# Kernel tuning notes

Measured on AMD Instinct MI355X. Metric: run time of the kernel, lower is better.

The kernel has to match this reference:

```python
import jax, jax.numpy as jnp
import numpy as np


def setup_inputs() -> dict:
    key = jax.random.key(0)
    k1, k2, k3, k4, k5 = jax.random.split(key, 5)
    B, Te, Td, De, Dd = 8, 256, 256, 512, 512
    return {
        "encoder_out_seq": jax.random.normal(k1, (B, Te, De), dtype=jnp.float32),
        "decoder_out_seq": jax.random.normal(k2, (B, Td, Dd), dtype=jnp.float32),
        "W_a": jax.random.normal(k3, (De, De), dtype=jnp.float32) * 0.05,
        "U_a": jax.random.normal(k4, (Dd, De), dtype=jnp.float32) * 0.05,
        "V_a": jax.random.normal(k5, (De, 1), dtype=jnp.float32) * 0.05,
    }


def reference(encoder_out_seq, decoder_out_seq, W_a, U_a, V_a):
    # Bahdanau additive attention, fully vectorized over decoder timesteps
    # (replaces the two sequential K.rnn scans in the original).
    Ws = jnp.einsum('bte,ef->btf', encoder_out_seq, W_a)   # [B,Te,De]
    Uh = jnp.einsum('bqd,df->bqf', decoder_out_seq, U_a)   # [B,Td,De]
    # scores[b,q,t] = tanh(Ws[b,t,:] + Uh[b,q,:]) . V_a
    scores = jnp.einsum('bqtf,f->bqt',
                        jnp.tanh(Ws[:, None, :, :] + Uh[:, :, None, :]),
                        V_a[:, 0])                          # [B,Td,Te]
    e = jax.nn.softmax(scores, axis=-1)                     # attention weights
    c = jnp.einsum('bqt,btf->bqf', e, encoder_out_seq)      # context vectors
    return (c, e)
```

## Files before the change

kernel.cpp:

```cpp
#include <hip/hip_runtime.h>

#define NB 8
#define TE 256
#define TD 256
#define DE 512
#define QT 4

#define K2SCALE 2.8853900817779268f

typedef short bf16x8 __attribute__((ext_vector_type(8)));
typedef float f32x4 __attribute__((ext_vector_type(4)));
typedef unsigned short u16x8 __attribute__((ext_vector_type(8)));

static __device__ __forceinline__ unsigned short f2bf(float x) {
  unsigned int u = __float_as_uint(x);
  u += 0x7fffu + ((u >> 16) & 1u);
  return (unsigned short)(u >> 16);
}

static __device__ __forceinline__ void split8(
    const float4& x0, const float4& x1, u16x8& h, u16x8& l) {
  float xs[8] = {x0.x, x0.y, x0.z, x0.w, x1.x, x1.y, x1.z, x1.w};
  #pragma unroll
  for (int j = 0; j < 8; ++j) {
    unsigned short hh = f2bf(xs[j]);
    float hf = __uint_as_float((unsigned int)hh << 16);
    h[j] = hh;
    l[j] = f2bf(xs[j] - hf);
  }
}

__global__ __launch_bounds__(256) void convB(
    const float* __restrict__ w0, unsigned short* __restrict__ h0, unsigned short* __restrict__ l0,
    const float* __restrict__ w1, unsigned short* __restrict__ h1, unsigned short* __restrict__ l1)
{
  const float* W = blockIdx.z ? w1 : w0;
  unsigned short* H = blockIdx.z ? h1 : h0;
  unsigned short* L = blockIdx.z ? l1 : l0;
  __shared__ unsigned short sh[32][33], sl[32][33];
  const int t = threadIdx.x;
  const int k0 = blockIdx.y * 32, n0 = blockIdx.x * 32;
  const int r = t >> 3, c = (t & 7) * 4;
  float4 x = *(const float4*)(W + (size_t)(k0 + r) * DE + n0 + c);
  float xs[4] = {x.x, x.y, x.z, x.w};
  #pragma unroll
  for (int j = 0; j < 4; ++j) {
    unsigned short hh = f2bf(xs[j]);
    float hf = __uint_as_float((unsigned int)hh << 16);
    sh[r][c + j] = hh;
    sl[r][c + j] = f2bf(xs[j] - hf);
  }
  __syncthreads();
  ushort4 oh, ol;
  oh.x = sh[c + 0][r]; oh.y = sh[c + 1][r]; oh.z = sh[c + 2][r]; oh.w = sh[c + 3][r];
  ol.x = sl[c + 0][r]; ol.y = sl[c + 1][r]; ol.z = sl[c + 2][r]; ol.w = sl[c + 3][r];
  *(ushort4*)(H + (size_t)(n0 + r) * DE + k0 + c) = oh;
  *(ushort4*)(L + (size_t)(n0 + r) * DE + k0 + c) = ol;
}

__global__ __launch_bounds__(256) void gemm_mfma(
    const float* __restrict__ A0,
    const unsigned short* __restrict__ BH0, const unsigned short* __restrict__ BL0,
    float* __restrict__ C0,
    const float* __restrict__ A1,
    const unsigned short* __restrict__ BH1, const unsigned short* __restrict__ BL1,
    float* __restrict__ C1)
{
  const int blk = blockIdx.x;
  const int xcd = blk & 7;
  const int j = blk >> 3;
  const int panel = xcd * 8 + (j & 7);
  const int bx = j >> 3;
  const int by = panel & 31;
  const int bz = panel >> 5;
  const float*          A  = bz ? A1  : A0;
  const unsigned short* BH = bz ? BH1 : BH0;
  const unsigned short* BL = bz ? BL1 : BL0;
  float*                C  = bz ? C1  : C0;
  const int tid  = threadIdx.x;
  const int lane = tid & 63;
  const int wave = tid >> 6;
  const int wm = wave >> 1, wn = wave & 1;
  const int g = lane >> 4, r16 = lane & 15;
  const int m0 = by * 64, n0 = bx * 64;
  __shared__ __align__(16) unsigned short Ah[2][64][40], Al[2][64][40];
  __shared__ __align__(16) unsigned short Bh[2][64][40], Bl[2][64][40];
  const int arow = tid >> 2;
  const int apart = (tid & 3) * 8;

  float4 a00, a01;
  u16x8 pb, plb;
#define LOADTILE(KT) do {                                                   \
    const size_t ko = (size_t)(KT) * 32 + apart;                            \
    const float* pa_ = A + (size_t)(m0 + arow) * 512 + ko;                  \
    a00 = *(const float4*)pa_;  a01 = *(const float4*)(pa_ + 4);            \
    pb  = *(const u16x8*)(BH + (size_t)(n0 + arow) * 512 + ko);             \
    plb = *(const u16x8*)(BL + (size_t)(n0 + arow) * 512 + ko);             \
  } while (0)
#define STORETILE(BUF) do {                                                 \
    u16x8 h0_, l0_;                                                         \
    split8(a00, a01, h0_, l0_);                                             \
    *(u16x8*)&Ah[BUF][arow][apart] = h0_;                                   \
    *(u16x8*)&Al[BUF][arow][apart] = l0_;                                   \
    *(u16x8*)&Bh[BUF][arow][apart] = pb;                                    \
    *(u16x8*)&Bl[BUF][arow][apart] = plb;                                   \
  } while (0)

  f32x4 accm[2][2], acce[2][2];
  #pragma unroll
  for (int mt = 0; mt < 2; ++mt)
    #pragma unroll
    for (int nt = 0; nt < 2; ++nt) {
      accm[mt][nt] = (f32x4){0.f, 0.f, 0.f, 0.f};
      acce[mt][nt] = (f32x4){0.f, 0.f, 0.f, 0.f};
    }

  LOADTILE(0);
  STORETILE(0);
  __syncthreads();

  for (int kt = 0; kt < 16; ++kt) {
    const int cur = kt & 1;
    if (kt + 1 < 16) LOADTILE(kt + 1);
    bf16x8 ah[2], al[2], bh[2], bl[2];
    #pragma unroll
    for (int mt = 0; mt < 2; ++mt) {
      ah[mt] = *(const bf16x8*)&Ah[cur][wm * 32 + mt * 16 + r16][g * 8];
      al[mt] = *(const bf16x8*)&Al[cur][wm * 32 + mt * 16 + r16][g * 8];
    }
    #pragma unroll
    for (int nt = 0; nt < 2; ++nt) {
      bh[nt] = *(const bf16x8*)&Bh[cur][wn * 32 + nt * 16 + r16][g * 8];
      bl[nt] = *(const bf16x8*)&Bl[cur][wn * 32 + nt * 16 + r16][g * 8];
    }
    #pragma unroll
    for (int mt = 0; mt < 2; ++mt)
      #pragma unroll
      for (int nt = 0; nt < 2; ++nt) {
        accm[mt][nt] = __builtin_amdgcn_mfma_f32_16x16x32_bf16(ah[mt], bh[nt], accm[mt][nt], 0, 0, 0);
        acce[mt][nt] = __builtin_amdgcn_mfma_f32_16x16x32_bf16(al[mt], bh[nt], acce[mt][nt], 0, 0, 0);
        acce[mt][nt] = __builtin_amdgcn_mfma_f32_16x16x32_bf16(ah[mt], bl[nt], acce[mt][nt], 0, 0, 0);
      }
    if (kt + 1 < 16) STORETILE(cur ^ 1);
    __syncthreads();
  }
#undef LOADTILE
#undef STORETILE

  #pragma unroll
  for (int mt = 0; mt < 2; ++mt)
    #pragma unroll
    for (int nt = 0; nt < 2; ++nt)
      #pragma unroll
      for (int jj = 0; jj < 4; ++jj) {
        float vsum = accm[mt][nt][jj] + acce[mt][nt][jj];
        int row = m0 + wm * 32 + mt * 16 + g * 4 + jj;
        int col = n0 + wn * 32 + nt * 16 + r16;
        C[(size_t)row * 512 + col] = __builtin_amdgcn_exp2f(vsum * K2SCALE);
      }
}

__global__ __launch_bounds__(512) void attn(
    const float* __restrict__ ws, const float* __restrict__ uh,
    const float* __restrict__ enc, const float* __restrict__ va,
    float* __restrict__ out_c, float* __restrict__ out_e)
{
  const int tid  = threadIdx.x;
  const int wave = tid >> 6;
  const int lane = tid & 63;
  const int b  = blockIdx.x & 7;
  const int q0 = (blockIdx.x >> 3) * QT;
  __shared__ float s_sc[QT][TE];
  __shared__ float red[3][QT][DE];
  const int fbase = lane * 8;

  float4 v0 = *(const float4*)(va + fbase);
  float4 v1 = *(const float4*)(va + fbase + 4);
  float v[8] = {v0.x, v0.y, v0.z, v0.w, v1.x, v1.y, v1.z, v1.w};

  float eu[QT][8];
  #pragma unroll
  for (int q = 0; q < QT; ++q) {
    const float* up = uh + (size_t)(b * TD + q0 + q) * DE + fbase;
    float4 u0 = *(const float4*)(up);
    float4 u1 = *(const float4*)(up + 4);
    eu[q][0] = u0.x; eu[q][1] = u0.y; eu[q][2] = u0.z; eu[q][3] = u0.w;
    eu[q][4] = u1.x; eu[q][5] = u1.y; eu[q][6] = u1.z; eu[q][7] = u1.w;
  }

  const int t0 = wave * 32;
  const float* wp = ws + (size_t)(b * TE + t0) * DE + fbase;
  float4 w0 = *(const float4*)(wp);
  float4 w1 = *(const float4*)(wp + 4);
  for (int t = t0; t < t0 + 32; ++t) {
    float cw[8] = {w0.x, w0.y, w0.z, w0.w, w1.x, w1.y, w1.z, w1.w};
    wp += DE;
    w0 = *(const float4*)(wp);
    w1 = *(const float4*)(wp + 4);
    float a[QT];
    #pragma unroll
    for (int q = 0; q < QT; ++q) {
      float A0 = fmaf(cw[0], eu[q][0], 1.f);
      float A1 = fmaf(cw[1], eu[q][1], 1.f);
      float A2 = fmaf(cw[2], eu[q][2], 1.f);
      float A3 = fmaf(cw[3], eu[q][3], 1.f);
      float B0 = fmaf(cw[4], eu[q][4], 1.f);
      float B1 = fmaf(cw[5], eu[q][5], 1.f);
      float B2 = fmaf(cw[6], eu[q][6], 1.f);
      float B3 = fmaf(cw[7], eu[q][7], 1.f);
      float n1 = fmaf(v[1], A0, v[0] * A1);
      float d1 = A0 * A1;
      float n2 = fmaf(v[3], A2, v[2] * A3);
      float d2 = A2 * A3;
      float N1 = fmaf(n2, d1, n1 * d2);
      float D1 = d1 * d2;
      float n3 = fmaf(v[5], B0, v[4] * B1);
      float d3 = B0 * B1;
      float n4 = fmaf(v[7], B2, v[6] * B3);
      float d4 = B2 * B3;
      float N2 = fmaf(n4, d3, n3 * d4);
      float D2 = d3 * d4;
      float s = N1 * __builtin_amdgcn_rcpf(D1);
      a[q] = fmaf(N2, __builtin_amdgcn_rcpf(D2), s);
    }
    {
      const bool h1 = lane & 1;
      float m0 = h1 ? a[1] : a[0], o0 = h1 ? a[0] : a[1];
      float m1 = h1 ? a[3] : a[2], o1 = h1 ? a[2] : a[3];
      float r0 = m0 + __shfl_xor(o0, 1, 64);
      float r1 = m1 + __shfl_xor(o1, 1, 64);
      const bool h2 = lane & 2;
      float mm = h2 ? r1 : r0, oo = h2 ? r0 : r1;
      float r = mm + __shfl_xor(oo, 2, 64);
      r += __shfl_xor(r, 4, 64);
      r += __shfl_xor(r, 8, 64);
      r += __shfl_xor(r, 16, 64);
      r += __shfl_xor(r, 32, 64);
      if (lane < QT) s_sc[lane][t] = -2.f * r;
    }
  }
  __syncthreads();

  if (wave < QT) {
    const int r = wave;
    float x[4];
    #pragma unroll
    for (int i = 0; i < 4; ++i) x[i] = s_sc[r][lane + 64 * i];
    float m = fmaxf(fmaxf(x[0], x[1]), fmaxf(x[2], x[3]));
    #pragma unroll
    for (int off = 32; off >= 1; off >>= 1) m = fmaxf(m, __shfl_xor(m, off, 64));
    const float L2E = 1.4426950408889634f;
    float ssum = 0.f;
    #pragma unroll
    for (int i = 0; i < 4; ++i) { x[i] = __builtin_amdgcn_exp2f((x[i] - m) * L2E); ssum += x[i]; }
    #pragma unroll
    for (int off = 32; off >= 1; off >>= 1) ssum += __shfl_xor(ssum, off, 64);
    float inv = 1.f / ssum;
    float* oe = out_e + (size_t)(b * TD + q0 + r) * TE;
    #pragma unroll
    for (int i = 0; i < 4; ++i) {
      float e = x[i] * inv;
      s_sc[r][lane + 64 * i] = e;
      oe[lane + 64 * i] = e;
    }
  }
  __syncthreads();

  {
    const int fgrp = tid >> 7;
    const int f4   = (tid & 127) * 4;
    float4 c[QT];
    #pragma unroll
    for (int q = 0; q < QT; ++q) c[q] = make_float4(0.f, 0.f, 0.f, 0.f);
    const float* eb = enc + (size_t)b * TE * DE + f4;
    const int tb = fgrp * 64;
    #pragma unroll 4
    for (int t = tb; t < tb + 64; ++t) {
      float4 ee = *(const float4*)(eb + (size_t)t * DE);
      #pragma unroll
      for (int q = 0; q < QT; ++q) {
        float w = s_sc[q][t];
        c[q].x = fmaf(w, ee.x, c[q].x);
        c[q].y = fmaf(w, ee.y, c[q].y);
        c[q].z = fmaf(w, ee.z, c[q].z);
        c[q].w = fmaf(w, ee.w, c[q].w);
      }
    }
    if (fgrp > 0) {
      #pragma unroll
      for (int q = 0; q < QT; ++q) *(float4*)&red[fgrp - 1][q][f4] = c[q];
    }
    __syncthreads();
    if (fgrp == 0) {
      #pragma unroll
      for (int q = 0; q < QT; ++q) {
        float4 r1 = *(const float4*)&red[0][q][f4];
        float4 r2 = *(const float4*)&red[1][q][f4];
        float4 r3 = *(const float4*)&red[2][q][f4];
        c[q].x += (r1.x + r2.x) + r3.x;
        c[q].y += (r1.y + r2.y) + r3.y;
        c[q].z += (r1.z + r2.z) + r3.z;
        c[q].w += (r1.w + r2.w) + r3.w;
        *(float4*)(out_c + (size_t)(b * TD + q0 + q) * DE + f4) = c[q];
      }
    }
  }
}

extern "C" void kernel_launch(void* const* d_in, const int* in_sizes, int n_in,
                              void* d_out, int out_size, void* d_ws, size_t ws_size,
                              hipStream_t stream) {
  const float* enc = (const float*)d_in[0];
  const float* dec = (const float*)d_in[1];
  const float* Wa  = (const float*)d_in[2];
  const float* Ua  = (const float*)d_in[3];
  const float* Va  = (const float*)d_in[4];
  float* out_c = (float*)d_out;
  float* out_e = out_c + (size_t)NB * TD * DE;

  float* ws = (float*)d_ws;
  float* uh = ws + 1048576;
  unsigned short* BHw = (unsigned short*)(uh + 1048576);
  unsigned short* BLw = BHw + 262144;
  unsigned short* BHu = BLw + 262144;
  unsigned short* BLu = BHu + 262144;

  convB<<<dim3(16, 16, 2), dim3(256), 0, stream>>>(Wa, BHw, BLw, Ua, BHu, BLu);
  gemm_mfma<<<dim3(512), dim3(256), 0, stream>>>(
      enc, BHw, BLw, ws, dec, BHu, BLu, uh);
  attn<<<dim3(NB * (TD / QT)), dim3(512), 0, stream>>>(
      ws, uh, enc, Va, out_c, out_e);
}
```

Measured before the change: 68.72 us.

## Split fused attention kernel into separate score and softmax/context kernels

The fused attn kernel becomes two kernels. The first computes the additive-attention scores with four times as many smaller blocks (256 threads, 16 timesteps per wave) and writes them to a global workspace buffer. The second reads those scores, then does the softmax and the context product. This raises parallelism for the tanh-heavy score phase at the cost of an extra launch and a global round trip for the score matrix.

```diff
diff --git a/kernel.cpp b/kernel.cpp
--- a/kernel.cpp
+++ b/kernel.cpp
@@ -160,18 +160,19 @@
       }
 }
 
-__global__ __launch_bounds__(512) void attn(
+__global__ __launch_bounds__(256) void scores(
     const float* __restrict__ ws, const float* __restrict__ uh,
-    const float* __restrict__ enc, const float* __restrict__ va,
-    float* __restrict__ out_c, float* __restrict__ out_e)
+    const float* __restrict__ va, float* __restrict__ out_s)
 {
   const int tid  = threadIdx.x;
   const int wave = tid >> 6;
   const int lane = tid & 63;
-  const int b  = blockIdx.x & 7;
-  const int q0 = (blockIdx.x >> 3) * QT;
-  __shared__ float s_sc[QT][TE];
-  __shared__ float red[3][QT][DE];
+  const int blk  = blockIdx.x;
+  const int b    = blk & 7;
+  const int rest = blk >> 3;
+  const int q0   = (rest & 63) * QT;
+  const int tt   = rest >> 6;
+  const int t0   = tt * 64 + wave * 16;
   const int fbase = lane * 8;
 
   float4 v0 = *(const float4*)(va + fbase);
@@ -188,11 +189,10 @@
     eu[q][4] = u1.x; eu[q][5] = u1.y; eu[q][6] = u1.z; eu[q][7] = u1.w;
   }
 
-  const int t0 = wave * 32;
   const float* wp = ws + (size_t)(b * TE + t0) * DE + fbase;
   float4 w0 = *(const float4*)(wp);
   float4 w1 = *(const float4*)(wp + 4);
-  for (int t = t0; t < t0 + 32; ++t) {
+  for (int t = t0; t < t0 + 16; ++t) {
     float cw[8] = {w0.x, w0.y, w0.z, w0.w, w1.x, w1.y, w1.z, w1.w};
     wp += DE;
     w0 = *(const float4*)(wp);
@@ -236,16 +236,30 @@
       r += __shfl_xor(r, 8, 64);
       r += __shfl_xor(r, 16, 64);
       r += __shfl_xor(r, 32, 64);
-      if (lane < QT) s_sc[lane][t] = -2.f * r;
-    }
-  }
-  __syncthreads();
+      if (lane < QT)
+        out_s[(size_t)(b * TD + q0 + lane) * TE + t] = -2.f * r;
+    }
+  }
+}
+
+__global__ __launch_bounds__(512) void attn2(
+    const float* __restrict__ gs, const float* __restrict__ enc,
+    float* __restrict__ out_c, float* __restrict__ out_e)
+{
+  const int tid  = threadIdx.x;
+  const int wave = tid >> 6;
+  const int lane = tid & 63;
+  const int b  = blockIdx.x & 7;
+  const int q0 = (blockIdx.x >> 3) * QT;
+  __shared__ float s_sc[QT][TE];
+  __shared__ float red[3][QT][DE];
 
   if (wave < QT) {
     const int r = wave;
+    const float* row = gs + (size_t)(b * TD + q0 + r) * TE;
     float x[4];
     #pragma unroll
-    for (int i = 0; i < 4; ++i) x[i] = s_sc[r][lane + 64 * i];
+    for (int i = 0; i < 4; ++i) x[i] = row[lane + 64 * i];
     float m = fmaxf(fmaxf(x[0], x[1]), fmaxf(x[2], x[3]));
     #pragma unroll
     for (int off = 32; off >= 1; off >>= 1) m = fmaxf(m, __shfl_xor(m, off, 64));
@@ -324,10 +338,11 @@
   unsigned short* BLw = BHw + 262144;
   unsigned short* BHu = BLw + 262144;
   unsigned short* BLu = BHu + 262144;
+  float* gsc = (float*)(BLu + 262144);
 
   convB<<<dim3(16, 16, 2), dim3(256), 0, stream>>>(Wa, BHw, BLw, Ua, BHu, BLu);
   gemm_mfma<<<dim3(512), dim3(256), 0, stream>>>(
       enc, BHw, BLw, ws, dec, BHu, BLu, uh);
-  attn<<<dim3(NB * (TD / QT)), dim3(512), 0, stream>>>(
-      ws, uh, enc, Va, out_c, out_e);
-}
+  scores<<<dim3(NB * (TD / QT) * 4), dim3(256), 0, stream>>>(ws, uh, Va, gsc);
+  attn2<<<dim3(NB * (TD / QT)), dim3(512), 0, stream>>>(gsc, enc, out_c, out_e);
+}
```

Result: slower. 73.27 us (+6.6%).
